# Performance work log

Hardware: AMD Instinct MI355X
Metric: run time of the kernel (lower is better)

The kernel has to match this reference:

```python
import jax, jax.numpy as jnp
import numpy as np

MARGIN = 0.5
SCALE = 64.0
EPS = 1e-12  # matches torch F.normalize default eps


def setup_inputs() -> dict:
    key = jax.random.key(0)
    k1, k2, k3 = jax.random.split(key, 3)
    B, D, C = 1024, 512, 100000
    features = jax.random.normal(k1, (B, D), dtype=jnp.float32)
    labels = jax.random.randint(k2, (B,), 0, C, dtype=jnp.int64)
    # xavier_uniform for [C, D] weight: bound = sqrt(6/(C+D))
    bound = np.sqrt(6.0 / (C + D)).astype(np.float32)
    weight = jax.random.uniform(k3, (C, D), dtype=jnp.float32, minval=-bound, maxval=bound)
    return {"features": features, "labels": labels, "weight": weight}


def _l2norm(x):
    # F.normalize(dim=1): x / max(||x||, eps)
    n = jnp.sqrt(jnp.sum(x * x, axis=1, keepdims=True))
    return x / jnp.maximum(n, EPS)


def reference(features, labels, weight):
    f = _l2norm(features)              # [B, D]
    w = _l2norm(weight)                # [C, D]
    cos_theta = f @ w.T                # [B, C]
    B = features.shape[0]
    rows = jnp.arange(B)
    # subtract margin at the label position only (no one-hot materialization)
    cos_m = cos_theta.at[rows, labels].add(-MARGIN)
    logits = cos_m * SCALE
    logZ = jax.nn.logsumexp(logits, axis=1)        # [B]
    tgt = logits[rows, labels]                     # [B]
    loss = jnp.mean(logZ - tgt)
    return loss
```

## Files before the change

### kernel.cpp

```cpp
#include <hip/hip_runtime.h>
#include <hip/hip_bf16.h>
#include <hip/hip_fp8.h>
#include <stdint.h>

#define B_ROWS 1024
#define DIM    512
#define C_CLS  100000
#define C_PAD  100352
#define NT     784
#define NT_PER_XCD 98
#define MT     8
#define NPAD   (C_PAD - C_CLS)

using f32x4 = __attribute__((ext_vector_type(4))) float;
using i32x4 = __attribute__((ext_vector_type(4))) int;
using i32x8 = __attribute__((ext_vector_type(8))) int;

#define AS1(p) ((const __attribute__((address_space(1))) uint32_t*)(p))
#define AS3(p) ((__attribute__((address_space(3))) uint32_t*)(p))
#define SBAR()   __builtin_amdgcn_s_barrier()
#define VMCNT0() asm volatile("s_waitcnt vmcnt(0)" ::: "memory")

static __device__ __forceinline__ uint32_t f2fp8(float f) {
    __hip_fp8_e4m3 q(f);
    return (uint32_t)q.__x;
}
static __device__ __forceinline__ float fp82f(uint32_t b) {
    __hip_fp8_e4m3 h;
    h.__x = (__hip_fp8_storage_t)b;
    return (float)h;
}

__global__ __launch_bounds__(256) void normalize_rows(
    const float* __restrict__ src, uint8_t* __restrict__ dst, int nvalid, int ntotal)
{
    const int row  = blockIdx.x * 4 + (threadIdx.x >> 6);
    const int lane = threadIdx.x & 63;
    if (row >= ntotal) return;
    uint2* d2 = reinterpret_cast<uint2*>(dst + (size_t)row * DIM);
    if (row >= nvalid) { d2[lane] = make_uint2(0u, 0u); return; }
    const float4* s4 = reinterpret_cast<const float4*>(src + (size_t)row * DIM);
    const float4 a = s4[lane * 2], b = s4[lane * 2 + 1];
    float ss = a.x*a.x + a.y*a.y + a.z*a.z + a.w*a.w
             + b.x*b.x + b.y*b.y + b.z*b.z + b.w*b.w;
    #pragma unroll
    for (int k = 1; k < 64; k <<= 1) ss += __shfl_xor(ss, k);
    const float inv = 1.0f / fmaxf(sqrtf(ss), 1e-12f);
    uint2 o;
    o.x = f2fp8(a.x*inv) | (f2fp8(a.y*inv) << 8) | (f2fp8(a.z*inv) << 16) | (f2fp8(a.w*inv) << 24);
    o.y = f2fp8(b.x*inv) | (f2fp8(b.y*inv) << 8) | (f2fp8(b.z*inv) << 16) | (f2fp8(b.w*inv) << 24);
    d2[lane] = o;
}

__global__ __launch_bounds__(256, 3) void gemm_lse(
    const uint8_t* __restrict__ A,
    const uint8_t* __restrict__ W,
    float* __restrict__ ps)
{
    __shared__ __align__(16) uint8_t lds[2][128 * 128];

    const int tid  = threadIdx.x;
    const int lane = tid & 63;
    const int wid  = tid >> 6;
    const int wm   = wid >> 1;
    const int wn   = wid & 1;

    const int b     = blockIdx.x;
    const int xcd   = b & 7;
    const int j     = b >> 3;
    const int ntile = xcd * NT_PER_XCD + (j >> 3);
    const int mtile = j & 7;

    const uint8_t* Abase = A + (size_t)mtile * 128 * DIM;
    const uint8_t* Bbase = W + (size_t)ntile * 128 * DIM;

    auto stage = [&](int kt) {
        #pragma unroll
        for (int p = 0; p < 4; ++p) {
            const int u   = tid + p * 256;
            const int row = u >> 3;
            const int sub = (u & 7) ^ (row & 7);
            const uint8_t* As = Abase + (size_t)row * DIM + kt * 128 + sub * 16;
            const uint8_t* Bs = Bbase + (size_t)row * DIM + kt * 128 + sub * 16;
            __builtin_amdgcn_global_load_lds(AS1(As), AS3(&lds[0][u * 16]), 16, 0, 0);
            __builtin_amdgcn_global_load_lds(AS1(Bs), AS3(&lds[1][u * 16]), 16, 0, 0);
        }
    };

    const int l15 = lane & 15;
    const int uhi = lane >> 4;

    i32x8 aF[4], bF[4];
    f32x4 acc[4][4] = {};

    auto ldfrag = [&](const uint8_t* base, int row) -> i32x8 {
        const int swz = row & 7;
        const i32x4 lo = *reinterpret_cast<const i32x4*>(base + row * 128 + (((uhi << 1) | 0) ^ swz) * 16);
        const i32x4 hi = *reinterpret_cast<const i32x4*>(base + row * 128 + (((uhi << 1) | 1) ^ swz) * 16);
        i32x8 r;
        r[0] = lo[0]; r[1] = lo[1]; r[2] = lo[2]; r[3] = lo[3];
        r[4] = hi[0]; r[5] = hi[1]; r[6] = hi[2]; r[7] = hi[3];
        return r;
    };

    stage(0);

    #pragma unroll 1
    for (int kt = 0; kt < 4; ++kt) {
        VMCNT0(); SBAR();
        #pragma unroll
        for (int mi = 0; mi < 4; ++mi) aF[mi] = ldfrag(&lds[0][0], wm * 64 + mi * 16 + l15);
        #pragma unroll
        for (int ni = 0; ni < 4; ++ni) bF[ni] = ldfrag(&lds[1][0], wn * 64 + ni * 16 + l15);
        #pragma unroll
        for (int mi = 0; mi < 4; ++mi)
            #pragma unroll
            for (int ni = 0; ni < 4; ++ni)
                acc[mi][ni] = __builtin_amdgcn_mfma_scale_f32_16x16x128_f8f6f4(
                    aF[mi], bF[ni], acc[mi][ni], 0, 0, 0, 127, 0, 127);
        SBAR();
        if (kt < 3) stage(kt + 1);
    }

    __syncthreads();
    float* red = reinterpret_cast<float*>(&lds[0][0]);
    #pragma unroll
    for (int mi = 0; mi < 4; ++mi) {
        #pragma unroll
        for (int r = 0; r < 4; ++r) {
            float s = __expf(fmaf(acc[mi][0][r], 64.0f, -64.0f))
                    + __expf(fmaf(acc[mi][1][r], 64.0f, -64.0f))
                    + __expf(fmaf(acc[mi][2][r], 64.0f, -64.0f))
                    + __expf(fmaf(acc[mi][3][r], 64.0f, -64.0f));
            #pragma unroll
            for (int k = 1; k < 16; k <<= 1) s += __shfl_xor(s, k);
            if (l15 == 0) red[(wm * 64 + mi * 16 + uhi * 4 + r) * 2 + wn] = s;
        }
    }
    __syncthreads();
    if (tid < 128)
        ps[(size_t)ntile * B_ROWS + mtile * 128 + tid] = red[tid * 2] + red[tid * 2 + 1];
}

__global__ __launch_bounds__(256) void finalize(
    const float* __restrict__ ps,
    const uint8_t* __restrict__ fb, const uint8_t* __restrict__ wb,
    const int* __restrict__ labels, float* __restrict__ row_loss)
{
    const int row = blockIdx.x;
    const int t   = threadIdx.x;
    const int lab = labels[row];

    const uint8_t* frow = fb + (size_t)row * DIM;
    const uint8_t* wrow = wb + (size_t)lab * DIM;
    uint32_t fa = *reinterpret_cast<const uint16_t*>(frow + 2 * t);
    uint32_t wa = *reinterpret_cast<const uint16_t*>(wrow + 2 * t);
    float d = fp82f(fa & 0xffu) * fp82f(wa & 0xffu)
            + fp82f(fa >> 8)    * fp82f(wa >> 8);
    #pragma unroll
    for (int k = 1; k < 64; k <<= 1) d += __shfl_xor(d, k);

    float s = 0.0f;
    for (int i = t; i < NT; i += 256) s += ps[(size_t)i * B_ROWS + row];
    #pragma unroll
    for (int k = 1; k < 64; k <<= 1) s += __shfl_xor(s, k);

    __shared__ float sd[4], ssm[4];
    if ((t & 63) == 0) { sd[t >> 6] = d; ssm[t >> 6] = s; }
    __syncthreads();
    if (t == 0) {
        const float dt = sd[0] + sd[1] + sd[2] + sd[3];
        float S = ssm[0] + ssm[1] + ssm[2] + ssm[3];
        const float lt = 64.0f * dt;
        S += expf(lt - 96.0f) - expf(lt - 64.0f) - (float)NPAD * expf(-64.0f);
        row_loss[row] = 64.0f + logf(S) - (lt - 32.0f);
    }
}

__global__ __launch_bounds__(256) void mean_k(const float* __restrict__ rl, float* __restrict__ out)
{
    const int t = threadIdx.x;
    float s = 0.0f;
    for (int i = t; i < B_ROWS; i += 256) s += rl[i];
    #pragma unroll
    for (int k = 1; k < 64; k <<= 1) s += __shfl_xor(s, k);
    __shared__ float r4[4];
    if ((t & 63) == 0) r4[t >> 6] = s;
    __syncthreads();
    if (t == 0) out[0] = (r4[0] + r4[1] + r4[2] + r4[3]) * (1.0f / B_ROWS);
}

extern "C" void kernel_launch(void* const* d_in, const int* in_sizes, int n_in,
                              void* d_out, int out_size, void* d_ws, size_t ws_size,
                              hipStream_t stream)
{
    const float* features = (const float*)d_in[0];
    const int*   labels   = (const int*)d_in[1];
    const float* weight   = (const float*)d_in[2];

    char* ws = (char*)d_ws;
    uint8_t* wb = (uint8_t*)ws;
    uint8_t* fb = (uint8_t*)(ws + (size_t)C_PAD * DIM);
    float*   psum = (float*)(ws + (size_t)C_PAD * DIM + (size_t)B_ROWS * DIM);
    float*   rl = psum + (size_t)NT * B_ROWS;

    normalize_rows<<<C_PAD / 4, 256, 0, stream>>>(weight, wb, C_CLS, C_PAD);
    normalize_rows<<<B_ROWS / 4, 256, 0, stream>>>(features, fb, B_ROWS, B_ROWS);
    gemm_lse<<<NT * MT, 256, 0, stream>>>(fb, wb, psum);
    finalize<<<B_ROWS, 256, 0, stream>>>(psum, fb, wb, labels, rl);
    mean_k<<<1, 256, 0, stream>>>(rl, (float*)d_out);
}
```

Baseline: 129.7 us.

## Double-buffer LDS and register fragments in fp8 GEMM K-loop

```diff
diff --git a/kernel.cpp b/kernel.cpp
--- a/kernel.cpp
+++ b/kernel.cpp
@@ -19,6 +19,8 @@
 #define AS1(p) ((const __attribute__((address_space(1))) uint32_t*)(p))
 #define AS3(p) ((__attribute__((address_space(3))) uint32_t*)(p))
 #define SBAR()   __builtin_amdgcn_s_barrier()
+#define SCHED0() __builtin_amdgcn_sched_barrier(0)
+#define LGKM0()  asm volatile("s_waitcnt lgkmcnt(0)" ::: "memory")
 #define VMCNT0() asm volatile("s_waitcnt vmcnt(0)" ::: "memory")
 
 static __device__ __forceinline__ uint32_t f2fp8(float f) {
@@ -52,12 +54,12 @@
     d2[lane] = o;
 }
 
-__global__ __launch_bounds__(256, 3) void gemm_lse(
+__global__ __launch_bounds__(256, 2) void gemm_lse(
     const uint8_t* __restrict__ A,
     const uint8_t* __restrict__ W,
     float* __restrict__ ps)
 {
-    __shared__ __align__(16) uint8_t lds[2][128 * 128];
+    __shared__ __align__(16) uint8_t lds[2][2][128 * 128];
 
     const int tid  = threadIdx.x;
     const int lane = tid & 63;
@@ -74,7 +76,7 @@
     const uint8_t* Abase = A + (size_t)mtile * 128 * DIM;
     const uint8_t* Bbase = W + (size_t)ntile * 128 * DIM;
 
-    auto stage = [&](int kt) {
+    auto stage = [&](int kt, int buf) {
         #pragma unroll
         for (int p = 0; p < 4; ++p) {
             const int u   = tid + p * 256;
@@ -82,19 +84,20 @@
             const int sub = (u & 7) ^ (row & 7);
             const uint8_t* As = Abase + (size_t)row * DIM + kt * 128 + sub * 16;
             const uint8_t* Bs = Bbase + (size_t)row * DIM + kt * 128 + sub * 16;
-            __builtin_amdgcn_global_load_lds(AS1(As), AS3(&lds[0][u * 16]), 16, 0, 0);
-            __builtin_amdgcn_global_load_lds(AS1(Bs), AS3(&lds[1][u * 16]), 16, 0, 0);
+            __builtin_amdgcn_global_load_lds(AS1(As), AS3(&lds[buf][0][u * 16]), 16, 0, 0);
+            __builtin_amdgcn_global_load_lds(AS1(Bs), AS3(&lds[buf][1][u * 16]), 16, 0, 0);
         }
     };
 
     const int l15 = lane & 15;
     const int uhi = lane >> 4;
 
-    i32x8 aF[4], bF[4];
+    i32x8 aF[2][4], bF[2][4];
     f32x4 acc[4][4] = {};
 
-    auto ldfrag = [&](const uint8_t* base, int row) -> i32x8 {
+    auto ldfrag = [&](int buf, int reg, int row) -> i32x8 {
         const int swz = row & 7;
+        const uint8_t* base = &lds[buf][reg][0];
         const i32x4 lo = *reinterpret_cast<const i32x4*>(base + row * 128 + (((uhi << 1) | 0) ^ swz) * 16);
         const i32x4 hi = *reinterpret_cast<const i32x4*>(base + row * 128 + (((uhi << 1) | 1) ^ swz) * 16);
         i32x8 r;
@@ -103,27 +106,37 @@
         return r;
     };
 
-    stage(0);
-
-    #pragma unroll 1
+    stage(0, 0);
+    VMCNT0(); SBAR();
+    #pragma unroll
+    for (int mi = 0; mi < 4; ++mi) aF[0][mi] = ldfrag(0, 0, wm * 64 + mi * 16 + l15);
+    #pragma unroll
+    for (int ni = 0; ni < 4; ++ni) bF[0][ni] = ldfrag(0, 1, wn * 64 + ni * 16 + l15);
+    stage(1, 1);
+
+    #pragma unroll
     for (int kt = 0; kt < 4; ++kt) {
-        VMCNT0(); SBAR();
-        #pragma unroll
-        for (int mi = 0; mi < 4; ++mi) aF[mi] = ldfrag(&lds[0][0], wm * 64 + mi * 16 + l15);
-        #pragma unroll
-        for (int ni = 0; ni < 4; ++ni) bF[ni] = ldfrag(&lds[1][0], wn * 64 + ni * 16 + l15);
+        const int cur = kt & 1, nxt = cur ^ 1;
+        LGKM0(); SCHED0();
+        VMCNT0();
+        SBAR();
+        if (kt < 3) {
+            #pragma unroll
+            for (int mi = 0; mi < 4; ++mi) aF[nxt][mi] = ldfrag(nxt, 0, wm * 64 + mi * 16 + l15);
+            #pragma unroll
+            for (int ni = 0; ni < 4; ++ni) bF[nxt][ni] = ldfrag(nxt, 1, wn * 64 + ni * 16 + l15);
+        }
+        if (kt < 2) stage(kt + 2, cur);
         #pragma unroll
         for (int mi = 0; mi < 4; ++mi)
             #pragma unroll
             for (int ni = 0; ni < 4; ++ni)
                 acc[mi][ni] = __builtin_amdgcn_mfma_scale_f32_16x16x128_f8f6f4(
-                    aF[mi], bF[ni], acc[mi][ni], 0, 0, 0, 127, 0, 127);
-        SBAR();
-        if (kt < 3) stage(kt + 1);
+                    aF[cur][mi], bF[cur][ni], acc[mi][ni], 0, 0, 0, 127, 0, 127);
     }
 
     __syncthreads();
-    float* red = reinterpret_cast<float*>(&lds[0][0]);
+    float* red = reinterpret_cast<float*>(&lds[0][0][0]);
     #pragma unroll
     for (int mi = 0; mi < 4; ++mi) {
         #pragma unroll
```

New measurement: 155.1 us. 19.5% more time.
